# Kernel optimization log

Measured on AMD Instinct MI355X. Metric: run time of the kernel, lower is better.

## Reference

```python
import jax, jax.numpy as jnp
import numpy as np

N_NODES = 50000
N_EDGES = 800000
N_REL = 16
D = 64          # entity_dim == relation_dim == n_hidden
NEG_SLOPE = 0.01  # torch F.leaky_relu default


def setup_inputs() -> dict:
    key = jax.random.key(0)
    ks = jax.random.split(key, 12)
    s = 1.0 / np.sqrt(D)
    return {
        "node_ids": jnp.arange(N_NODES, dtype=jnp.int64) if jax.config.jax_enable_x64 else jnp.arange(N_NODES, dtype=jnp.int32),
        "relation_ids": jax.random.randint(ks[0], (N_EDGES,), 0, N_REL),
        "src": jax.random.randint(ks[1], (N_EDGES,), 0, N_NODES),
        "dst": jax.random.randint(ks[2], (N_EDGES,), 0, N_NODES),
        "entity_embed": jax.random.normal(ks[3], (N_NODES, D), jnp.float32) * s,
        "relation_embed": jax.random.normal(ks[4], (N_REL, D), jnp.float32) * s,
        "W0": jax.random.normal(ks[5], (N_REL, D, D), jnp.float32) * s,
        "W1": jax.random.normal(ks[6], (N_REL, D, D), jnp.float32) * s,
        "ra0": jax.random.normal(ks[7], (D, D), jnp.float32) * s,
        "rb0": jax.random.normal(ks[8], (D, D), jnp.float32) * s,
        "ra1": jax.random.normal(ks[9], (D, D), jnp.float32) * s,
        "rb1": jax.random.normal(ks[10], (D, D), jnp.float32) * s,
    }


def _edge_softmax(scores, dst, n_nodes):
    # segment softmax over edges grouped by destination node (DGL edge_softmax)
    m = jax.ops.segment_max(scores, dst, num_segments=n_nodes)  # [N]
    e = jnp.exp(scores - m[dst])                                # [E]
    z = jax.ops.segment_sum(e, dst, num_segments=n_nodes)       # [N]
    return e / z[dst]


def _kgat_layer(h, efeat, src, dst, etype, Wr, ra, rb, n_nodes):
    # transform every node under every relation once: [N, R, Dr]
    trans = jnp.einsum('nd,rde->nre', h, Wr)
    t_r = trans[src, etype]                   # W_r h_t  [E, Dr]
    h_r = trans[dst, etype]                   # W_r h_h  [E, Dr]
    att = jnp.sum(t_r * jnp.tanh(h_r + efeat), axis=1)  # [E]
    a = _edge_softmax(att, dst, n_nodes)                 # [E]
    # u_mul_e + sum: scatter-add weighted source features to dst
    h_nb = jax.ops.segment_sum(h[src] * a[:, None], dst, num_segments=n_nodes)
    # Bi residual
    out = (jax.nn.leaky_relu((h + h_nb) @ ra, NEG_SLOPE)
           + jax.nn.leaky_relu((h * h_nb) @ rb, NEG_SLOPE))
    return out


def reference(node_ids, relation_ids, src, dst, entity_embed, relation_embed,
              W0, W1, ra0, rb0, ra1, rb1):
    h = entity_embed[node_ids]                 # [N, D]
    efeat = relation_embed[relation_ids]       # [E, D]
    n_nodes = node_ids.shape[0]
    cache = [h]
    for Wr, ra, rb in ((W0, ra0, rb0), (W1, ra1, rb1)):
        h = _kgat_layer(h, efeat, src, dst, relation_ids, Wr, ra, rb, n_nodes)
        cache.append(h)
    return jnp.concatenate(cache, axis=1)      # [N, 3*D]
```

## Files before the change

### kernel.cpp

```cpp
#include <hip/hip_runtime.h>
#include <hip/hip_bf16.h>
#include <math.h>

#define NN 50000
#define NE 800000
#define NR 16
#define DD 64
#define OSTRIDE 192

typedef __attribute__((ext_vector_type(8))) short bf16x8;
typedef __attribute__((ext_vector_type(4))) float f32x4;

__device__ inline float tanh_fast(float x) {
    return 1.f - 2.f / (__expf(2.f * x) + 1.f);
}
__device__ inline unsigned short f2bf(float f) {
    unsigned u = __float_as_uint(f);
    return (unsigned short)((u + 0x7fffu + ((u >> 16) & 1u)) >> 16);
}
__device__ inline float bf2f(unsigned short s) {
    return __uint_as_float((unsigned)s << 16);
}

__global__ void k_deg(const int* __restrict__ dst, const int* __restrict__ rel,
                      int* __restrict__ cnt, int* __restrict__ relmask) {
    for (int e = blockIdx.x * blockDim.x + threadIdx.x; e < NE;
         e += gridDim.x * blockDim.x) {
        int d = dst[e];
        atomicAdd(&cnt[d], 1);
        if (relmask) atomicOr(&relmask[d], 1 << rel[e]);
    }
}

__global__ __launch_bounds__(256) void k_scan1(const int* __restrict__ cnt,
                                               int* __restrict__ rowptr,
                                               int* __restrict__ bsum) {
    __shared__ int sh[256];
    int b = blockIdx.x, t = threadIdx.x;
    int i = b * 256 + t;
    int v = (i < NN) ? cnt[i] : 0;
    sh[t] = v;
    __syncthreads();
    #pragma unroll
    for (int o = 1; o < 256; o <<= 1) {
        int u = (t >= o) ? sh[t - o] : 0;
        __syncthreads();
        sh[t] += u;
        __syncthreads();
    }
    if (i < NN) rowptr[i] = sh[t] - v;
    if (t == 255) bsum[b] = sh[255];
}

__global__ __launch_bounds__(256) void k_scan2(int* __restrict__ bsum, int nb) {
    __shared__ int sh[256];
    int t = threadIdx.x;
    int v = (t < nb) ? bsum[t] : 0;
    sh[t] = v;
    __syncthreads();
    #pragma unroll
    for (int o = 1; o < 256; o <<= 1) {
        int u = (t >= o) ? sh[t - o] : 0;
        __syncthreads();
        sh[t] += u;
        __syncthreads();
    }
    if (t < nb) bsum[t] = sh[t] - v;
}

__global__ __launch_bounds__(256) void k_scan3(int* __restrict__ rowptr,
                                               const int* __restrict__ bsum,
                                               int* __restrict__ cursor) {
    int b = blockIdx.x, t = threadIdx.x;
    int i = b * 256 + t;
    if (i < NN) {
        int v = rowptr[i] + bsum[b];
        rowptr[i] = v;
        cursor[i] = v;
    }
    if (i == 0) rowptr[NN] = NE;
}

__global__ void k_fill(const int* __restrict__ dst, const int* __restrict__ src,
                       const int* __restrict__ rel, int* __restrict__ cursor,
                       int* __restrict__ epack) {
    for (int e = blockIdx.x * blockDim.x + threadIdx.x; e < NE;
         e += gridDim.x * blockDim.x) {
        int pos = atomicAdd(&cursor[dst[e]], 1);
        epack[pos] = src[e] | (rel[e] << 16);
    }
}

__global__ void k_copy_h0(const int* __restrict__ node_ids,
                          const float* __restrict__ ent,
                          float* __restrict__ out,
                          unsigned short* __restrict__ hbf) {
    int i = blockIdx.x * blockDim.x + threadIdx.x;
    if (i >= NN * DD) return;
    int n = i >> 6, d = i & 63;
    float v = ent[(size_t)node_ids[n] * DD + d];
    out[(size_t)n * OSTRIDE + d] = v;
    hbf[(size_t)n * DD + d] = f2bf(v);
}

__global__ void k_wprep(const float* __restrict__ W, unsigned short* __restrict__ wbf,
                        unsigned short* __restrict__ wtbf) {
    int i = blockIdx.x * blockDim.x + threadIdx.x;
    if (i >= NR * DD * DD) return;
    int r = i >> 12, rem = i & 4095, d = rem >> 6, E = rem & 63;
    unsigned short v = f2bf(W[i]);
    wbf[i] = v;
    wtbf[(r << 12) | (E << 6) | d] = v;
}

__global__ __launch_bounds__(256) void k_transq4(const unsigned short* __restrict__ hbf,
                                                 const unsigned short* __restrict__ wbf,
                                                 const unsigned short* __restrict__ wtbf,
                                                 const float* __restrict__ relE,
                                                 const int* __restrict__ relmask,
                                                 unsigned short* __restrict__ qbf) {
    __shared__ __align__(16) unsigned short u_lds[4][32][72];
    int r  = blockIdx.x;
    int n0 = blockIdx.y * 128;
    int t  = threadIdx.x;
    int w  = t >> 6, l = t & 63;
    int l15 = l & 15, lg = l >> 4;
    int base = n0 + w * 32;

    int ar0 = base + l15;      if (ar0 >= NN) ar0 = NN - 1;
    int ar1 = base + 16 + l15; if (ar1 >= NN) ar1 = NN - 1;
    const unsigned short* ap0 = hbf + (size_t)ar0 * DD + lg * 8;
    const unsigned short* ap1 = hbf + (size_t)ar1 * DD + lg * 8;
    bf16x8 a00 = *(const bf16x8*)ap0;
    bf16x8 a01 = *(const bf16x8*)(ap0 + 32);
    bf16x8 a10 = *(const bf16x8*)ap1;
    bf16x8 a11 = *(const bf16x8*)(ap1 + 32);

    f32x4 acc[2][4];
    #pragma unroll
    for (int ti = 0; ti < 2; ++ti)
        #pragma unroll
        for (int nt = 0; nt < 4; ++nt) acc[ti][nt] = (f32x4){0.f, 0.f, 0.f, 0.f};

    const unsigned short* wtr = wtbf + (r << 12);
    #pragma unroll
    for (int nt = 0; nt < 4; ++nt) {
        const unsigned short* bp = wtr + (nt * 16 + l15) * DD + lg * 8;
        bf16x8 b0 = *(const bf16x8*)bp;
        bf16x8 b1 = *(const bf16x8*)(bp + 32);
        acc[0][nt] = __builtin_amdgcn_mfma_f32_16x16x32_bf16(a00, b0, acc[0][nt], 0, 0, 0);
        acc[0][nt] = __builtin_amdgcn_mfma_f32_16x16x32_bf16(a01, b1, acc[0][nt], 0, 0, 0);
        acc[1][nt] = __builtin_amdgcn_mfma_f32_16x16x32_bf16(a10, b0, acc[1][nt], 0, 0, 0);
        acc[1][nt] = __builtin_amdgcn_mfma_f32_16x16x32_bf16(a11, b1, acc[1][nt], 0, 0, 0);
    }

    #pragma unroll
    for (int nt = 0; nt < 4; ++nt) {
        int E = nt * 16 + l15;
        float er = relE[r * DD + E];
        #pragma unroll
        for (int ti = 0; ti < 2; ++ti)
            #pragma unroll
            for (int reg = 0; reg < 4; ++reg)
                u_lds[w][ti * 16 + lg * 4 + reg][E] = f2bf(tanh_fast(acc[ti][nt][reg] + er));
    }
    asm volatile("s_waitcnt lgkmcnt(0)" ::: "memory");

    const unsigned short* up0 = &u_lds[w][l15][lg * 8];
    const unsigned short* up1 = &u_lds[w][16 + l15][lg * 8];
    bf16x8 u00 = *(const bf16x8*)up0;
    bf16x8 u01 = *(const bf16x8*)(up0 + 32);
    bf16x8 u10 = *(const bf16x8*)up1;
    bf16x8 u11 = *(const bf16x8*)(up1 + 32);

    f32x4 q4[2][4];
    #pragma unroll
    for (int ti = 0; ti < 2; ++ti)
        #pragma unroll
        for (int nt = 0; nt < 4; ++nt) q4[ti][nt] = (f32x4){0.f, 0.f, 0.f, 0.f};

    const unsigned short* wr = wbf + (r << 12);
    #pragma unroll
    for (int nt = 0; nt < 4; ++nt) {
        const unsigned short* bp = wr + (nt * 16 + l15) * DD + lg * 8;
        bf16x8 b0 = *(const bf16x8*)bp;
        bf16x8 b1 = *(const bf16x8*)(bp + 32);
        q4[0][nt] = __builtin_amdgcn_mfma_f32_16x16x32_bf16(u00, b0, q4[0][nt], 0, 0, 0);
        q4[0][nt] = __builtin_amdgcn_mfma_f32_16x16x32_bf16(u01, b1, q4[0][nt], 0, 0, 0);
        q4[1][nt] = __builtin_amdgcn_mfma_f32_16x16x32_bf16(u10, b0, q4[1][nt], 0, 0, 0);
        q4[1][nt] = __builtin_amdgcn_mfma_f32_16x16x32_bf16(u11, b1, q4[1][nt], 0, 0, 0);
    }

    #pragma unroll
    for (int ti = 0; ti < 2; ++ti) {
        #pragma unroll
        for (int reg = 0; reg < 4; ++reg) {
            int node = base + ti * 16 + lg * 4 + reg;
            if (node < NN) {
                int msk = relmask ? relmask[node] : 0xffff;
                if ((msk >> r) & 1) {
                    unsigned short* qp = qbf + ((size_t)node * NR + r) * DD + l15;
                    #pragma unroll
                    for (int nt = 0; nt < 4; ++nt)
                        qp[nt * 16] = f2bf(q4[ti][nt][reg]);
                }
            }
        }
    }
}

__global__ __launch_bounds__(256) void k_fused4(const unsigned short* __restrict__ qbf,
                                                const unsigned short* __restrict__ hbf,
                                                const int* __restrict__ rowptr,
                                                const int* __restrict__ epack,
                                                float* __restrict__ h_nb) {
    __shared__ __align__(16) unsigned short q_lds[4][1024];
    int wv = threadIdx.x >> 6;
    int n = blockIdx.x * 4 + wv;
    if (n >= NN) return;
    int lane = threadIdx.x & 63;

    {
        const uint4* s4 = (const uint4*)(qbf + (size_t)n * NR * DD);
        uint4* d4 = (uint4*)q_lds[wv];
        d4[lane]      = s4[lane];
        d4[lane + 64] = s4[lane + 64];
    }
    asm volatile("s_waitcnt vmcnt(0) lgkmcnt(0)" ::: "memory");

    int row0 = rowptr[n], deg = rowptr[n + 1] - row0;
    const unsigned short* ql = q_lds[wv];

    float m = -__builtin_inff(), zr = 0.f, acc = 0.f;
    bool s0 = lane & 1, s1 = lane & 2, s2 = lane & 4;

    int i = 0;
    for (; i + 8 <= deg; i += 8) {
        float v[8], hv[8];
        #pragma unroll
        for (int j = 0; j < 8; ++j) {
            int p = epack[row0 + i + j];
            int s = p & 0xffff, r = p >> 16;
            hv[j] = bf2f(hbf[(size_t)s * DD + lane]);
            v[j]  = hv[j] * bf2f(ql[r * DD + lane]);
        }
        float x0 = s0 ? v[1] : v[0], o0 = s0 ? v[0] : v[1];
        float x1 = s0 ? v[3] : v[2], o1 = s0 ? v[2] : v[3];
        float x2 = s0 ? v[5] : v[4], o2 = s0 ? v[4] : v[5];
        float x3 = s0 ? v[7] : v[6], o3 = s0 ? v[6] : v[7];
        x0 += __shfl_xor(o0, 1, 64);
        x1 += __shfl_xor(o1, 1, 64);
        x2 += __shfl_xor(o2, 1, 64);
        x3 += __shfl_xor(o3, 1, 64);
        float y0 = s1 ? x1 : x0, p0 = s1 ? x0 : x1;
        float y1 = s1 ? x3 : x2, p1 = s1 ? x2 : x3;
        y0 += __shfl_xor(p0, 2, 64);
        y1 += __shfl_xor(p1, 2, 64);
        float sj = s2 ? y1 : y0, q0 = s2 ? y0 : y1;
        sj += __shfl_xor(q0, 4, 64);
        sj += __shfl_xor(sj, 8, 64);
        sj += __shfl_xor(sj, 16, 64);
        sj += __shfl_xor(sj, 32, 64);

        float cm = sj;
        cm = fmaxf(cm, __shfl_xor(cm, 1, 64));
        cm = fmaxf(cm, __shfl_xor(cm, 2, 64));
        cm = fmaxf(cm, __shfl_xor(cm, 4, 64));
        float mn = fmaxf(m, cm);
        float sc = __expf(m - mn);
        float wgt = __expf(sj - mn);
        float zn = wgt;
        zn += __shfl_xor(zn, 1, 64);
        zn += __shfl_xor(zn, 2, 64);
        zn += __shfl_xor(zn, 4, 64);
        zr = zr * sc + zn;
        acc *= sc;
        #pragma unroll
        for (int j = 0; j < 8; ++j)
            acc += __shfl(wgt, j, 8) * hv[j];
        m = mn;
    }
    for (; i < deg; ++i) {
        int p = epack[row0 + i];
        int s = p & 0xffff, r = p >> 16;
        float hsv = bf2f(hbf[(size_t)s * DD + lane]);
        float v = hsv * bf2f(ql[r * DD + lane]);
        #pragma unroll
        for (int o = 32; o; o >>= 1) v += __shfl_xor(v, o, 64);
        float mn = fmaxf(m, v);
        float sc = __expf(m - mn);
        float wgt = __expf(v - mn);
        zr  = zr * sc + wgt;
        acc = acc * sc + wgt * hsv;
        m = mn;
    }
    h_nb[(size_t)n * DD + lane] = (deg > 0) ? acc / zr : 0.f;
}

__global__ __launch_bounds__(256) void k_out2(const float* __restrict__ h_nb,
                                              const float* __restrict__ ra,
                                              const float* __restrict__ rb,
                                              float* __restrict__ out,
                                              int off_in, int off_out,
                                              unsigned short* __restrict__ hbf) {
    __shared__ __align__(16) float v1s[64][68];
    __shared__ __align__(16) float v2s[64][68];
    __shared__ __align__(16) float ws[2][64][64];
    int t = threadIdx.x;
    int n0 = blockIdx.x * 64;

    for (int i = t; i < 1024; i += 256) {
        int ni = i >> 4, c4 = (i & 15) * 4;
        int n = n0 + ni;
        float4 hv = make_float4(0.f, 0.f, 0.f, 0.f);
        float4 nb = make_float4(0.f, 0.f, 0.f, 0.f);
        if (n < NN) {
            hv = *(const float4*)&out[(size_t)n * OSTRIDE + off_in + c4];
            nb = *(const float4*)&h_nb[(size_t)n * DD + c4];
        }
        v1s[c4 + 0][ni] = hv.x + nb.x;  v2s[c4 + 0][ni] = hv.x * nb.x;
        v1s[c4 + 1][ni] = hv.y + nb.y;  v2s[c4 + 1][ni] = hv.y * nb.y;
        v1s[c4 + 2][ni] = hv.z + nb.z;  v2s[c4 + 2][ni] = hv.z * nb.z;
        v1s[c4 + 3][ni] = hv.w + nb.w;  v2s[c4 + 3][ni] = hv.w * nb.w;
    }
    for (int i = t; i < 2048; i += 256) {
        const float* base = (i < 1024) ? ra : rb;
        int rem = i & 1023;
        float4 v = *(const float4*)&base[rem * 4];
        int k = rem >> 4, c4 = (rem & 15) * 4;
        *(float4*)&ws[i >> 10][k][c4] = v;
    }
    __syncthreads();

    int nd0 = (t >> 4) * 4;
    int c0  = (t & 15) * 4;
    float a1[4][4] = {}, a2[4][4] = {};
    #pragma unroll 8
    for (int k = 0; k < 64; ++k) {
        float4 h1 = *(const float4*)&v1s[k][nd0];
        float4 h2 = *(const float4*)&v2s[k][nd0];
        float4 wa = *(const float4*)&ws[0][k][c0];
        float4 wb = *(const float4*)&ws[1][k][c0];
        float x1[4] = {h1.x, h1.y, h1.z, h1.w};
        float x2[4] = {h2.x, h2.y, h2.z, h2.w};
        #pragma unroll
        for (int i = 0; i < 4; ++i) {
            a1[i][0] += x1[i] * wa.x; a1[i][1] += x1[i] * wa.y;
            a1[i][2] += x1[i] * wa.z; a1[i][3] += x1[i] * wa.w;
            a2[i][0] += x2[i] * wb.x; a2[i][1] += x2[i] * wb.y;
            a2[i][2] += x2[i] * wb.z; a2[i][3] += x2[i] * wb.w;
        }
    }
    #pragma unroll
    for (int i = 0; i < 4; ++i) {
        int n = n0 + nd0 + i;
        if (n >= NN) continue;
        float4 o;
        float* po = (float*)&o;
        #pragma unroll
        for (int j = 0; j < 4; ++j) {
            float u1 = a1[i][j], u2 = a2[i][j];
            u1 = u1 > 0.f ? u1 : 0.01f * u1;
            u2 = u2 > 0.f ? u2 : 0.01f * u2;
            po[j] = u1 + u2;
        }
        *(float4*)&out[(size_t)n * OSTRIDE + off_out + c0] = o;
        hbf[(size_t)n * DD + c0 + 0] = f2bf(o.x);
        hbf[(size_t)n * DD + c0 + 1] = f2bf(o.y);
        hbf[(size_t)n * DD + c0 + 2] = f2bf(o.z);
        hbf[(size_t)n * DD + c0 + 3] = f2bf(o.w);
    }
}

extern "C" void kernel_launch(void* const* d_in, const int* in_sizes, int n_in,
                              void* d_out, int out_size, void* d_ws, size_t ws_size,
                              hipStream_t stream) {
    const int*   node_ids = (const int*)d_in[0];
    const int*   rel_ids  = (const int*)d_in[1];
    const int*   src      = (const int*)d_in[2];
    const int*   dst      = (const int*)d_in[3];
    const float* ent      = (const float*)d_in[4];
    const float* relE     = (const float*)d_in[5];
    const float* W[2]  = {(const float*)d_in[6], (const float*)d_in[7]};
    const float* ra[2] = {(const float*)d_in[8], (const float*)d_in[10]};
    const float* rb[2] = {(const float*)d_in[9], (const float*)d_in[11]};
    float* out = (float*)d_out;

    const size_t hnb_bytes    = (size_t)NN * DD * sizeof(float);
    const size_t qbf_bytes    = (size_t)NN * NR * DD * sizeof(short);
    const size_t hbf_bytes    = (size_t)NN * DD * sizeof(short);
    const size_t wbf_bytes    = (size_t)NR * DD * DD * sizeof(short);
    const size_t epack_bytes  = (size_t)NE * sizeof(int);
    const size_t rowptr_bytes = (size_t)(NN + 1) * sizeof(int);
    const size_t cnt_bytes    = (size_t)NN * sizeof(int);
    const size_t mask_bytes   = (size_t)NN * sizeof(int);
    const int    NB_SCAN      = (NN + 255) / 256;
    const size_t bsum_bytes   = (size_t)256 * sizeof(int);

    char* p = (char*)d_ws;
    float*          h_nb   = (float*)p;          p += hnb_bytes;
    unsigned short* qbf    = (unsigned short*)p; p += qbf_bytes;
    unsigned short* hbf    = (unsigned short*)p; p += hbf_bytes;
    unsigned short* wbf    = (unsigned short*)p; p += wbf_bytes;
    unsigned short* wtbf   = (unsigned short*)p; p += wbf_bytes;
    int*            epack  = (int*)p;            p += epack_bytes;
    int*            rowptr = (int*)p;            p += rowptr_bytes;
    int*            cnt    = (int*)p;            p += cnt_bytes;
    int*            bsum   = (int*)p;            p += bsum_bytes;
    size_t used = (size_t)(p - (char*)d_ws);
    int* relmask = (used + mask_bytes <= ws_size) ? (int*)p : nullptr;

    hipMemsetAsync(cnt, 0, cnt_bytes, stream);
    if (relmask) hipMemsetAsync(relmask, 0, mask_bytes, stream);
    k_deg  <<<1024, 256, 0, stream>>>(dst, rel_ids, cnt, relmask);
    k_scan1<<<NB_SCAN, 256, 0, stream>>>(cnt, rowptr, bsum);
    k_scan2<<<1, 256, 0, stream>>>(bsum, NB_SCAN);
    k_scan3<<<NB_SCAN, 256, 0, stream>>>(rowptr, bsum, cnt);
    k_fill <<<1024, 256, 0, stream>>>(dst, src, rel_ids, cnt, epack);

    k_copy_h0<<<(NN * DD + 255) / 256, 256, 0, stream>>>(node_ids, ent, out, hbf);

    dim3 tq_grid(NR, (NN + 127) / 128);
    for (int L = 0; L < 2; ++L) {
        int off_in = L * DD;
        int off_out = (L + 1) * DD;

        k_wprep <<<(NR * DD * DD + 255) / 256, 256, 0, stream>>>(W[L], wbf, wtbf);
        k_transq4<<<tq_grid, 256, 0, stream>>>(hbf, wbf, wtbf, relE, relmask, qbf);
        k_fused4<<<(NN + 3) / 4, 256, 0, stream>>>(qbf, hbf, rowptr, epack, h_nb);
        k_out2  <<<(NN + 63) / 64, 256, 0, stream>>>(h_nb, ra[L], rb[L], out,
                                                     off_in, off_out, hbf);
    }
}
```

Measured before the change: 447.7 us.

## Fuse per-node relation transform into edge softmax aggregation kernel via LDS

Merges the per-relation q computation (two MFMA GEMMs with tanh) into the edge aggregation kernel, so each block computes q for 16 nodes across all 16 relations into shared memory and then runs the online softmax over their incoming edges. This removes the global write and read of the large bf16 q buffer, along with the relation-mask atomics that tracked which relations each node needed. In exchange, every node now computes q for all relations, and the larger shared-memory footprint may reduce occupancy.

```diff
diff --git a/kernel.cpp b/kernel.cpp
--- a/kernel.cpp
+++ b/kernel.cpp
@@ -7,6 +7,7 @@
 #define NR 16
 #define DD 64
 #define OSTRIDE 192
+#define QSTRIDE 1032
 
 typedef __attribute__((ext_vector_type(8))) short bf16x8;
 typedef __attribute__((ext_vector_type(4))) float f32x4;
@@ -22,14 +23,10 @@
     return __uint_as_float((unsigned)s << 16);
 }
 
-__global__ void k_deg(const int* __restrict__ dst, const int* __restrict__ rel,
-                      int* __restrict__ cnt, int* __restrict__ relmask) {
+__global__ void k_deg(const int* __restrict__ dst, int* __restrict__ cnt) {
     for (int e = blockIdx.x * blockDim.x + threadIdx.x; e < NE;
-         e += gridDim.x * blockDim.x) {
-        int d = dst[e];
-        atomicAdd(&cnt[d], 1);
-        if (relmask) atomicOr(&relmask[d], 1 << rel[e]);
-    }
+         e += gridDim.x * blockDim.x)
+        atomicAdd(&cnt[dst[e]], 1);
 }
 
 __global__ __launch_bounds__(256) void k_scan1(const int* __restrict__ cnt,
@@ -113,188 +110,150 @@
     wtbf[(r << 12) | (E << 6) | d] = v;
 }
 
-__global__ __launch_bounds__(256) void k_transq4(const unsigned short* __restrict__ hbf,
-                                                 const unsigned short* __restrict__ wbf,
-                                                 const unsigned short* __restrict__ wtbf,
-                                                 const float* __restrict__ relE,
-                                                 const int* __restrict__ relmask,
-                                                 unsigned short* __restrict__ qbf) {
-    __shared__ __align__(16) unsigned short u_lds[4][32][72];
-    int r  = blockIdx.x;
-    int n0 = blockIdx.y * 128;
+__global__ __launch_bounds__(256) void k_fused5(const unsigned short* __restrict__ hbf,
+                                                const unsigned short* __restrict__ wbf,
+                                                const unsigned short* __restrict__ wtbf,
+                                                const float* __restrict__ relE,
+                                                const int* __restrict__ rowptr,
+                                                const int* __restrict__ epack,
+                                                float* __restrict__ h_nb) {
+    __shared__ __align__(16) unsigned short q_lds[16 * QSTRIDE];
+    __shared__ __align__(16) unsigned short u_lds[4][16][72];
+    int n0 = blockIdx.x * 16;
     int t  = threadIdx.x;
     int w  = t >> 6, l = t & 63;
     int l15 = l & 15, lg = l >> 4;
-    int base = n0 + w * 32;
-
-    int ar0 = base + l15;      if (ar0 >= NN) ar0 = NN - 1;
-    int ar1 = base + 16 + l15; if (ar1 >= NN) ar1 = NN - 1;
-    const unsigned short* ap0 = hbf + (size_t)ar0 * DD + lg * 8;
-    const unsigned short* ap1 = hbf + (size_t)ar1 * DD + lg * 8;
-    bf16x8 a00 = *(const bf16x8*)ap0;
-    bf16x8 a01 = *(const bf16x8*)(ap0 + 32);
-    bf16x8 a10 = *(const bf16x8*)ap1;
-    bf16x8 a11 = *(const bf16x8*)(ap1 + 32);
-
-    f32x4 acc[2][4];
-    #pragma unroll
-    for (int ti = 0; ti < 2; ++ti)
-        #pragma unroll
-        for (int nt = 0; nt < 4; ++nt) acc[ti][nt] = (f32x4){0.f, 0.f, 0.f, 0.f};
-
-    const unsigned short* wtr = wtbf + (r << 12);
-    #pragma unroll
-    for (int nt = 0; nt < 4; ++nt) {
-        const unsigned short* bp = wtr + (nt * 16 + l15) * DD + lg * 8;
-        bf16x8 b0 = *(const bf16x8*)bp;
-        bf16x8 b1 = *(const bf16x8*)(bp + 32);
-        acc[0][nt] = __builtin_amdgcn_mfma_f32_16x16x32_bf16(a00, b0, acc[0][nt], 0, 0, 0);
-        acc[0][nt] = __builtin_amdgcn_mfma_f32_16x16x32_bf16(a01, b1, acc[0][nt], 0, 0, 0);
-        acc[1][nt] = __builtin_amdgcn_mfma_f32_16x16x32_bf16(a10, b0, acc[1][nt], 0, 0, 0);
-        acc[1][nt] = __builtin_amdgcn_mfma_f32_16x16x32_bf16(a11, b1, acc[1][nt], 0, 0, 0);
-    }
-
-    #pragma unroll
-    for (int nt = 0; nt < 4; ++nt) {
-        int E = nt * 16 + l15;
-        float er = relE[r * DD + E];
-        #pragma unroll
-        for (int ti = 0; ti < 2; ++ti)
+
+    int ar = n0 + l15; if (ar >= NN) ar = NN - 1;
+    const unsigned short* ap = hbf + (size_t)ar * DD + lg * 8;
+    bf16x8 a0 = *(const bf16x8*)ap;
+    bf16x8 a1 = *(const bf16x8*)(ap + 32);
+
+    for (int rr = 0; rr < 4; ++rr) {
+        int r = w + rr * 4;
+
+        f32x4 acc[4];
+        #pragma unroll
+        for (int nt = 0; nt < 4; ++nt) acc[nt] = (f32x4){0.f, 0.f, 0.f, 0.f};
+        const unsigned short* wtr = wtbf + (r << 12);
+        #pragma unroll
+        for (int nt = 0; nt < 4; ++nt) {
+            const unsigned short* bp = wtr + (nt * 16 + l15) * DD + lg * 8;
+            bf16x8 b0 = *(const bf16x8*)bp;
+            bf16x8 b1 = *(const bf16x8*)(bp + 32);
+            acc[nt] = __builtin_amdgcn_mfma_f32_16x16x32_bf16(a0, b0, acc[nt], 0, 0, 0);
+            acc[nt] = __builtin_amdgcn_mfma_f32_16x16x32_bf16(a1, b1, acc[nt], 0, 0, 0);
+        }
+
+        #pragma unroll
+        for (int nt = 0; nt < 4; ++nt) {
+            int E = nt * 16 + l15;
+            float er = relE[r * DD + E];
             #pragma unroll
             for (int reg = 0; reg < 4; ++reg)
-                u_lds[w][ti * 16 + lg * 4 + reg][E] = f2bf(tanh_fast(acc[ti][nt][reg] + er));
-    }
-    asm volatile("s_waitcnt lgkmcnt(0)" ::: "memory");
-
-    const unsigned short* up0 = &u_lds[w][l15][lg * 8];
-    const unsigned short* up1 = &u_lds[w][16 + l15][lg * 8];
-    bf16x8 u00 = *(const bf16x8*)up0;
-    bf16x8 u01 = *(const bf16x8*)(up0 + 32);
-    bf16x8 u10 = *(const bf16x8*)up1;
-    bf16x8 u11 = *(const bf16x8*)(up1 + 32);
-
-    f32x4 q4[2][4];
-    #pragma unroll
-    for (int ti = 0; ti < 2; ++ti)
-        #pragma unroll
-        for (int nt = 0; nt < 4; ++nt) q4[ti][nt] = (f32x4){0.f, 0.f, 0.f, 0.f};
-
-    const unsigned short* wr = wbf + (r << 12);
-    #pragma unroll
-    for (int nt = 0; nt < 4; ++nt) {
-        const unsigned short* bp = wr + (nt * 16 + l15) * DD + lg * 8;
-        bf16x8 b0 = *(const bf16x8*)bp;
-        bf16x8 b1 = *(const bf16x8*)(bp + 32);
-        q4[0][nt] = __builtin_amdgcn_mfma_f32_16x16x32_bf16(u00, b0, q4[0][nt], 0, 0, 0);
-        q4[0][nt] = __builtin_amdgcn_mfma_f32_16x16x32_bf16(u01, b1, q4[0][nt], 0, 0, 0);
-        q4[1][nt] = __builtin_amdgcn_mfma_f32_16x16x32_bf16(u10, b0, q4[1][nt], 0, 0, 0);
-        q4[1][nt] = __builtin_amdgcn_mfma_f32_16x16x32_bf16(u11, b1, q4[1][nt], 0, 0, 0);
-    }
-
-    #pragma unroll
-    for (int ti = 0; ti < 2; ++ti) {
+                u_lds[w][lg * 4 + reg][E] = f2bf(tanh_fast(acc[nt][reg] + er));
+        }
+        asm volatile("s_waitcnt lgkmcnt(0)" ::: "memory");
+
+        const unsigned short* up = &u_lds[w][l15][lg * 8];
+        bf16x8 u0 = *(const bf16x8*)up;
+        bf16x8 u1 = *(const bf16x8*)(up + 32);
+
+        f32x4 q4[4];
+        #pragma unroll
+        for (int nt = 0; nt < 4; ++nt) q4[nt] = (f32x4){0.f, 0.f, 0.f, 0.f};
+        const unsigned short* wr = wbf + (r << 12);
+        #pragma unroll
+        for (int nt = 0; nt < 4; ++nt) {
+            const unsigned short* bp = wr + (nt * 16 + l15) * DD + lg * 8;
+            bf16x8 b0 = *(const bf16x8*)bp;
+            bf16x8 b1 = *(const bf16x8*)(bp + 32);
+            q4[nt] = __builtin_amdgcn_mfma_f32_16x16x32_bf16(u0, b0, q4[nt], 0, 0, 0);
+            q4[nt] = __builtin_amdgcn_mfma_f32_16x16x32_bf16(u1, b1, q4[nt], 0, 0, 0);
+        }
+
         #pragma unroll
         for (int reg = 0; reg < 4; ++reg) {
-            int node = base + ti * 16 + lg * 4 + reg;
-            if (node < NN) {
-                int msk = relmask ? relmask[node] : 0xffff;
-                if ((msk >> r) & 1) {
-                    unsigned short* qp = qbf + ((size_t)node * NR + r) * DD + l15;
-                    #pragma unroll
-                    for (int nt = 0; nt < 4; ++nt)
-                        qp[nt * 16] = f2bf(q4[ti][nt][reg]);
-                }
+            unsigned short* qp = q_lds + (lg * 4 + reg) * QSTRIDE + r * 64 + l15;
+            #pragma unroll
+            for (int nt = 0; nt < 4; ++nt)
+                qp[nt * 16] = f2bf(q4[nt][reg]);
+        }
+    }
+    __syncthreads();
+
+    int lane = l;
+    bool s0 = lane & 1, s1 = lane & 2, s2 = lane & 4;
+    for (int kk = 0; kk < 4; ++kk) {
+        int ni = (w << 2) + kk;
+        int n = n0 + ni;
+        if (n >= NN) continue;
+        const unsigned short* ql = q_lds + ni * QSTRIDE;
+        int row0 = rowptr[n], deg = rowptr[n + 1] - row0;
+
+        float m = -__builtin_inff(), zr = 0.f, acc = 0.f;
+        int i = 0;
+        for (; i + 8 <= deg; i += 8) {
+            float v[8], hv[8];
+            #pragma unroll
+            for (int j = 0; j < 8; ++j) {
+                int p = epack[row0 + i + j];
+                int s = p & 0xffff, r = p >> 16;
+                hv[j] = bf2f(hbf[(size_t)s * DD + lane]);
+                v[j]  = hv[j] * bf2f(ql[r * DD + lane]);
             }
-        }
-    }
-}
-
-__global__ __launch_bounds__(256) void k_fused4(const unsigned short* __restrict__ qbf,
-                                                const unsigned short* __restrict__ hbf,
-                                                const int* __restrict__ rowptr,
-                                                const int* __restrict__ epack,
-                                                float* __restrict__ h_nb) {
-    __shared__ __align__(16) unsigned short q_lds[4][1024];
-    int wv = threadIdx.x >> 6;
-    int n = blockIdx.x * 4 + wv;
-    if (n >= NN) return;
-    int lane = threadIdx.x & 63;
-
-    {
-        const uint4* s4 = (const uint4*)(qbf + (size_t)n * NR * DD);
-        uint4* d4 = (uint4*)q_lds[wv];
-        d4[lane]      = s4[lane];
-        d4[lane + 64] = s4[lane + 64];
-    }
-    asm volatile("s_waitcnt vmcnt(0) lgkmcnt(0)" ::: "memory");
-
-    int row0 = rowptr[n], deg = rowptr[n + 1] - row0;
-    const unsigned short* ql = q_lds[wv];
-
-    float m = -__builtin_inff(), zr = 0.f, acc = 0.f;
-    bool s0 = lane & 1, s1 = lane & 2, s2 = lane & 4;
-
-    int i = 0;
-    for (; i + 8 <= deg; i += 8) {
-        float v[8], hv[8];
-        #pragma unroll
-        for (int j = 0; j < 8; ++j) {
-            int p = epack[row0 + i + j];
+            float x0 = s0 ? v[1] : v[0], o0 = s0 ? v[0] : v[1];
+            float x1 = s0 ? v[3] : v[2], o1 = s0 ? v[2] : v[3];
+            float x2 = s0 ? v[5] : v[4], o2 = s0 ? v[4] : v[5];
+            float x3 = s0 ? v[7] : v[6], o3 = s0 ? v[6] : v[7];
+            x0 += __shfl_xor(o0, 1, 64);
+            x1 += __shfl_xor(o1, 1, 64);
+            x2 += __shfl_xor(o2, 1, 64);
+            x3 += __shfl_xor(o3, 1, 64);
+            float y0 = s1 ? x1 : x0, p0 = s1 ? x0 : x1;
+            float y1 = s1 ? x3 : x2, p1 = s1 ? x2 : x3;
+            y0 += __shfl_xor(p0, 2, 64);
+            y1 += __shfl_xor(p1, 2, 64);
+            float sj = s2 ? y1 : y0, q0 = s2 ? y0 : y1;
+            sj += __shfl_xor(q0, 4, 64);
+            sj += __shfl_xor(sj, 8, 64);
+            sj += __shfl_xor(sj, 16, 64);
+            sj += __shfl_xor(sj, 32, 64);
+
+            float cm = sj;
+            cm = fmaxf(cm, __shfl_xor(cm, 1, 64));
+            cm = fmaxf(cm, __shfl_xor(cm, 2, 64));
+            cm = fmaxf(cm, __shfl_xor(cm, 4, 64));
+            float mn = fmaxf(m, cm);
+            float sc = __expf(m - mn);
+            float wgt = __expf(sj - mn);
+            float zn = wgt;
+            zn += __shfl_xor(zn, 1, 64);
+            zn += __shfl_xor(zn, 2, 64);
+            zn += __shfl_xor(zn, 4, 64);
+            zr = zr * sc + zn;
+            acc *= sc;
+            #pragma unroll
+            for (int j = 0; j < 8; ++j)
+                acc += __shfl(wgt, j, 8) * hv[j];
+            m = mn;
+        }
+        for (; i < deg; ++i) {
+            int p = epack[row0 + i];
             int s = p & 0xffff, r = p >> 16;
-            hv[j] = bf2f(hbf[(size_t)s * DD + lane]);
-            v[j]  = hv[j] * bf2f(ql[r * DD + lane]);
-        }
-        float x0 = s0 ? v[1] : v[0], o0 = s0 ? v[0] : v[1];
-        float x1 = s0 ? v[3] : v[2], o1 = s0 ? v[2] : v[3];
-        float x2 = s0 ? v[5] : v[4], o2 = s0 ? v[4] : v[5];
-        float x3 = s0 ? v[7] : v[6], o3 = s0 ? v[6] : v[7];
-        x0 += __shfl_xor(o0, 1, 64);
-        x1 += __shfl_xor(o1, 1, 64);
-        x2 += __shfl_xor(o2, 1, 64);
-        x3 += __shfl_xor(o3, 1, 64);
-        float y0 = s1 ? x1 : x0, p0 = s1 ? x0 : x1;
-        float y1 = s1 ? x3 : x2, p1 = s1 ? x2 : x3;
-        y0 += __shfl_xor(p0, 2, 64);
-        y1 += __shfl_xor(p1, 2, 64);
-        float sj = s2 ? y1 : y0, q0 = s2 ? y0 : y1;
-        sj += __shfl_xor(q0, 4, 64);
-        sj += __shfl_xor(sj, 8, 64);
-        sj += __shfl_xor(sj, 16, 64);
-        sj += __shfl_xor(sj, 32, 64);
-
-        float cm = sj;
-        cm = fmaxf(cm, __shfl_xor(cm, 1, 64));
-        cm = fmaxf(cm, __shfl_xor(cm, 2, 64));
-        cm = fmaxf(cm, __shfl_xor(cm, 4, 64));
-        float mn = fmaxf(m, cm);
-        float sc = __expf(m - mn);
-        float wgt = __expf(sj - mn);
-        float zn = wgt;
-        zn += __shfl_xor(zn, 1, 64);
-        zn += __shfl_xor(zn, 2, 64);
-        zn += __shfl_xor(zn, 4, 64);
-        zr = zr * sc + zn;
-        acc *= sc;
-        #pragma unroll
-        for (int j = 0; j < 8; ++j)
-            acc += __shfl(wgt, j, 8) * hv[j];
-        m = mn;
-    }
-    for (; i < deg; ++i) {
-        int p = epack[row0 + i];
-        int s = p & 0xffff, r = p >> 16;
-        float hsv = bf2f(hbf[(size_t)s * DD + lane]);
-        float v = hsv * bf2f(ql[r * DD + lane]);
-        #pragma unroll
-        for (int o = 32; o; o >>= 1) v += __shfl_xor(v, o, 64);
-        float mn = fmaxf(m, v);
-        float sc = __expf(m - mn);
-        float wgt = __expf(v - mn);
-        zr  = zr * sc + wgt;
-        acc = acc * sc + wgt * hsv;
-        m = mn;
-    }
-    h_nb[(size_t)n * DD + lane] = (deg > 0) ? acc / zr : 0.f;
+            float hsv = bf2f(hbf[(size_t)s * DD + lane]);
+            float v = hsv * bf2f(ql[r * DD + lane]);
+            #pragma unroll
+            for (int o = 32; o; o >>= 1) v += __shfl_xor(v, o, 64);
+            float mn = fmaxf(m, v);
+            float sc = __expf(m - mn);
+            float wgt = __expf(v - mn);
+            zr  = zr * sc + wgt;
+            acc = acc * sc + wgt * hsv;
+            m = mn;
+        }
+        h_nb[(size_t)n * DD + lane] = (deg > 0) ? acc / zr : 0.f;
+    }
 }
 
 __global__ __launch_bounds__(256) void k_out2(const float* __restrict__ h_nb,
@@ -387,19 +346,16 @@
     float* out = (float*)d_out;
 
     const size_t hnb_bytes    = (size_t)NN * DD * sizeof(float);
-    const size_t qbf_bytes    = (size_t)NN * NR * DD * sizeof(short);
     const size_t hbf_bytes    = (size_t)NN * DD * sizeof(short);
     const size_t wbf_bytes    = (size_t)NR * DD * DD * sizeof(short);
     const size_t epack_bytes  = (size_t)NE * sizeof(int);
     const size_t rowptr_bytes = (size_t)(NN + 1) * sizeof(int);
     const size_t cnt_bytes    = (size_t)NN * sizeof(int);
-    const size_t mask_bytes   = (size_t)NN * sizeof(int);
     const int    NB_SCAN      = (NN + 255) / 256;
     const size_t bsum_bytes   = (size_t)256 * sizeof(int);
 
     char* p = (char*)d_ws;
     float*          h_nb   = (float*)p;          p += hnb_bytes;
-    unsigned short* qbf    = (unsigned short*)p; p += qbf_bytes;
     unsigned short* hbf    = (unsigned short*)p; p += hbf_bytes;
     unsigned short* wbf    = (unsigned short*)p; p += wbf_bytes;
     unsigned short* wtbf   = (unsigned short*)p; p += wbf_bytes;
@@ -407,12 +363,10 @@
     int*            rowptr = (int*)p;            p += rowptr_bytes;
     int*            cnt    = (int*)p;            p += cnt_bytes;
     int*            bsum   = (int*)p;            p += bsum_bytes;
-    size_t used = (size_t)(p - (char*)d_ws);
-    int* relmask = (used + mask_bytes <= ws_size) ? (int*)p : nullptr;
+    (void)ws_size;
 
     hipMemsetAsync(cnt, 0, cnt_bytes, stream);
-    if (relmask) hipMemsetAsync(relmask, 0, mask_bytes, stream);
-    k_deg  <<<1024, 256, 0, stream>>>(dst, rel_ids, cnt, relmask);
+    k_deg  <<<1024, 256, 0, stream>>>(dst, cnt);
     k_scan1<<<NB_SCAN, 256, 0, stream>>>(cnt, rowptr, bsum);
     k_scan2<<<1, 256, 0, stream>>>(bsum, NB_SCAN);
     k_scan3<<<NB_SCAN, 256, 0, stream>>>(rowptr, bsum, cnt);
@@ -420,14 +374,13 @@
 
     k_copy_h0<<<(NN * DD + 255) / 256, 256, 0, stream>>>(node_ids, ent, out, hbf);
 
-    dim3 tq_grid(NR, (NN + 127) / 128);
     for (int L = 0; L < 2; ++L) {
         int off_in = L * DD;
         int off_out = (L + 1) * DD;
 
         k_wprep <<<(NR * DD * DD + 255) / 256, 256, 0, stream>>>(W[L], wbf, wtbf);
-        k_transq4<<<tq_grid, 256, 0, stream>>>(hbf, wbf, wtbf, relE, relmask, qbf);
-        k_fused4<<<(NN + 3) / 4, 256, 0, stream>>>(qbf, hbf, rowptr, epack, h_nb);
+        k_fused5<<<(NN + 15) / 16, 256, 0, stream>>>(hbf, wbf, wtbf, relE,
+                                                     rowptr, epack, h_nb);
         k_out2  <<<(NN + 63) / 64, 256, 0, stream>>>(h_nb, ra[L], rb[L], out,
                                                      off_in, off_out, hbf);
     }
```

Measured after the change: 536.8 us. 19.9% more time.
